# Performance work log

Measured on AMD Instinct MI355X. Metric: run time of the kernel, lower is better.

Reference implementation:

```python
import jax, jax.numpy as jnp
import numpy as np

EPS = 1e-6

def _mlp3(x, Wa, ba, Wb, bb, Wc, bc):
    h = jax.nn.relu(x @ Wa + ba)
    h = jax.nn.relu(h @ Wb + bb)
    return h @ Wc + bc

def setup_inputs() -> dict:
    key = jax.random.key(0)
    ks = jax.random.split(key, 16)
    B, D, C, N = 1024, 1024, 128, 100000
    s = 0.02  # weight scale
    return {
        "query": jax.random.normal(ks[0], (B, D), jnp.float32),
        "W1": jax.random.normal(ks[1], (D, D // 2), jnp.float32) * s,
        "b1": jnp.zeros((D // 2,), jnp.float32),
        "W2": jax.random.normal(ks[2], (D // 2, D // 4), jnp.float32) * s,
        "b2": jnp.zeros((D // 4,), jnp.float32),
        "W3": jax.random.normal(ks[3], (D // 4, C), jnp.float32) * s,
        "b3": jnp.zeros((C,), jnp.float32),
        "keys": jax.random.normal(ks[4], (N, C), jnp.float32),
        "values": jax.random.normal(ks[5], (N, C), jnp.float32),
        "D1w": jax.random.normal(ks[6], (C, D // 4), jnp.float32) * s,
        "D1b": jnp.zeros((D // 4,), jnp.float32),
        "D2w": jax.random.normal(ks[7], (D // 4, D // 2), jnp.float32) * s,
        "D2b": jnp.zeros((D // 2,), jnp.float32),
        "D3w": jax.random.normal(ks[8], (D // 2, D), jnp.float32) * s,
        "D3b": jnp.zeros((D,), jnp.float32),
        "k": 5,
    }

def reference(query, W1, b1, W2, b2, W3, b3, keys, values,
              D1w, D1b, D2w, D2b, D3w, D3b, k):
    # Compress query (FAISS path detaches, so stop_gradient is faithful)
    cq = _mlp3(query, W1, b1, W2, b2, W3, b3)          # [B, C]
    cq = jax.lax.stop_gradient(cq)
    keys_c = jax.lax.stop_gradient(keys)
    vals = jax.lax.stop_gradient(values)               # stored values were .detach()ed
    # Brute-force squared-L2 distances (IndexFlatL2 returns squared L2): [B, N]
    d2 = (jnp.sum(cq * cq, axis=1, keepdims=True)
          + jnp.sum(keys_c * keys_c, axis=1)[None, :]
          - 2.0 * cq @ keys_c.T)
    neg_d, idx = jax.lax.top_k(-d2, k)                 # k nearest, ascending distance
    dist = -neg_d                                      # [B, k]
    w = 1.0 / (dist + EPS)
    w = w / jnp.sum(w, axis=1, keepdims=True)          # [B, k]
    gathered = vals[idx]                               # [B, k, C]
    weighted = jnp.einsum('bk,bkc->bc', w, gathered)   # [B, C]
    retrieved = _mlp3(weighted, D1w, D1b, D2w, D2b, D3w, D3b)  # [B, D]
    confidence = 1.0 / (dist[:, 0] + EPS)              # [B]
    return retrieved, confidence
```

## Files before the change

### kernel.cpp

```cpp
#include <hip/hip_runtime.h>
#include <hip/hip_bf16.h>

#define NKEYS  100000
#define NCH    128
#define CHK    832
#define TPC    13
#define KPAD   (NCH * CHK)
#define NTILE  (KPAD / 64)
#define BQ     1024
#define EPS_F  1e-6f
#define NCAND  (NCH * 3)
#define BIGF   1e30f

typedef __attribute__((ext_vector_type(8))) short bf16x8;
typedef __attribute__((ext_vector_type(4))) float f32x4;

__device__ __forceinline__ void gl_lds16(const uint4* g, uint4* l) {
    __builtin_amdgcn_global_load_lds((const __attribute__((address_space(1))) void*)g,
                                     (__attribute__((address_space(3))) void*)l, 16, 0, 0);
}
__device__ __forceinline__ unsigned umn(unsigned a, unsigned b) { return a < b ? a : b; }
__device__ __forceinline__ unsigned umx(unsigned a, unsigned b) { return a > b ? a : b; }
__device__ __forceinline__ ushort bf16bits(float v) {
    __hip_bfloat16 h = __float2bfloat16(v);
    return *(ushort*)&h;
}

__device__ __forceinline__ void ins3u(unsigned (&m)[3], unsigned u) {
    unsigned v1 = umn(m[2], u);
    m[2] = umx(m[1], v1);
    unsigned v2 = umn(m[1], v1);
    m[1] = umx(m[0], v2);
    m[0] = umn(m[0], v2);
}

__device__ __forceinline__ void ins5(float (&d)[5], int (&ix)[5], float nd, int ni) {
    if (nd < d[4]) {
        d[4] = nd; ix[4] = ni;
#pragma unroll
        for (int p = 4; p > 0; --p) {
            if (d[p] < d[p - 1]) {
                float td = d[p]; d[p] = d[p - 1]; d[p - 1] = td;
                int   ti = ix[p]; ix[p] = ix[p - 1]; ix[p - 1] = ti;
            }
        }
    }
}

__global__ __launch_bounds__(256)
void cvt_keys(const float* __restrict__ keys, uint4* __restrict__ img,
              float* __restrict__ kk, float* __restrict__ khalf) {
    const int tid = threadIdx.x;
    const int r = tid >> 2, s = tid & 3;
    const int tile = blockIdx.x;
    const int n = tile * 64 + r;
    const int ct = r >> 4, l15 = r & 15;
    const bool live = (n < NKEYS);
    const float* kp = keys + (size_t)n * 128 + s * 32;
    float ss = 0.f;
    uint4 out[4];
#pragma unroll
    for (int q = 0; q < 4; ++q) {
        float4 a = make_float4(0.f, 0.f, 0.f, 0.f), b = a;
        if (live) { a = *(const float4*)(kp + q * 8); b = *(const float4*)(kp + q * 8 + 4); }
        ss += a.x * a.x + a.y * a.y + a.z * a.z + a.w * a.w
            + b.x * b.x + b.y * b.y + b.z * b.z + b.w * b.w;
        float v[8] = {a.x, a.y, a.z, a.w, b.x, b.y, b.z, b.w};
        ushort h[8];
#pragma unroll
        for (int j = 0; j < 8; ++j) h[j] = bf16bits(v[j]);
        out[q] = make_uint4((uint)h[0] | ((uint)h[1] << 16), (uint)h[2] | ((uint)h[3] << 16),
                            (uint)h[4] | ((uint)h[5] << 16), (uint)h[6] | ((uint)h[7] << 16));
    }
    ss += __shfl_xor(ss, 1, 64);
    ss += __shfl_xor(ss, 2, 64);
    if (s == 0) {
        kk[n]    = live ? ss : BIGF;
        khalf[n] = live ? -0.5f * ss : -BIGF;
    }
#pragma unroll
    for (int q = 0; q < 4; ++q)
        img[(size_t)tile * 1024 + ((ct * 4 + s) * 4 + q) * 16 + l15] = out[q];
}

__global__ __launch_bounds__(256)
void split_a(const float* __restrict__ A, ushort* __restrict__ Ax, int K) {
    const int row = blockIdx.x;
    for (int i = threadIdx.x * 4; i < K; i += 1024) {
        float4 v = *(const float4*)&A[(size_t)row * K + i];
        float x[4] = {v.x, v.y, v.z, v.w};
        ushort h[4], l[4];
#pragma unroll
        for (int j = 0; j < 4; ++j) {
            __hip_bfloat16 hb = __float2bfloat16(x[j]);
            h[j] = *(ushort*)&hb;
            l[j] = bf16bits(x[j] - __bfloat162float(hb));
        }
        ushort* o = Ax + (size_t)row * 3 * K;
        *(ushort4*)&o[i]         = make_ushort4(h[0], h[1], h[2], h[3]);
        *(ushort4*)&o[K + i]     = make_ushort4(l[0], l[1], l[2], l[3]);
        *(ushort4*)&o[2 * K + i] = make_ushort4(h[0], h[1], h[2], h[3]);
    }
}

__global__ __launch_bounds__(256)
void cvt_wT_split(const float* __restrict__ W, uint4* __restrict__ Wimg,
                  int Ksrc, int N) {
    const int ctile = blockIdx.x, p = blockIdx.y;
    const int npanT = gridDim.y;
    const int pk = Ksrc >> 6;
    const int part = p / pk, psrc = p - part * pk;
#pragma unroll
    for (int it = 0; it < 2; ++it) {
        int c = it * 256 + threadIdx.x;
        int l15 = c & 15, quad = (c >> 4) & 3, s = (c >> 6) & 1, ct = c >> 7;
        int n = ctile * 64 + ct * 16 + l15;
        int k = psrc * 64 + s * 32 + quad * 8;
        ushort h[8];
#pragma unroll
        for (int j = 0; j < 8; ++j) {
            float w = W[(size_t)(k + j) * N + n];
            __hip_bfloat16 hb = __float2bfloat16(w);
            if (part < 2) h[j] = *(ushort*)&hb;
            else h[j] = bf16bits(w - __bfloat162float(hb));
        }
        Wimg[((size_t)ctile * npanT + p) * 512 + c] =
            make_uint4((uint)h[0] | ((uint)h[1] << 16), (uint)h[2] | ((uint)h[3] << 16),
                       (uint)h[4] | ((uint)h[5] << 16), (uint)h[6] | ((uint)h[7] << 16));
    }
}

__global__ __launch_bounds__(256)
void bgemm_part(const ushort* __restrict__ Abf, const uint4* __restrict__ Wimg,
                float* __restrict__ P, int M, int N, int K, int ppz) {
    __shared__ uint4 pan[2][512];
    const int tid = threadIdx.x;
    const int wv = tid >> 6, ln = tid & 63;
    const int quad = ln >> 4, l15 = ln & 15;
    const int n0 = blockIdx.x * 64;
    const int m0 = blockIdx.y * 128 + wv * 32;
    const int ctile = blockIdx.x, npanT = K >> 6;
    const int p0 = blockIdx.z * ppz;
    f32x4 acc[2][4];
#pragma unroll
    for (int s = 0; s < 2; ++s)
#pragma unroll
        for (int c = 0; c < 4; ++c) acc[s][c] = (f32x4){0.f, 0.f, 0.f, 0.f};

#pragma unroll
    for (int it = 0; it < 2; ++it)
        gl_lds16(&Wimg[((size_t)ctile * npanT + p0) * 512 + it * 256 + wv * 64 + ln],
                 &pan[0][it * 256 + wv * 64]);
    __syncthreads();

    for (int pp = 0; pp < ppz; ++pp) {
        const int p = p0 + pp;
        const int b = pp & 1;
        if (pp + 1 < ppz) {
#pragma unroll
            for (int it = 0; it < 2; ++it)
                gl_lds16(&Wimg[((size_t)ctile * npanT + p + 1) * 512 + it * 256 + wv * 64 + ln],
                         &pan[b ^ 1][it * 256 + wv * 64]);
        }
        const ushort* arow = Abf + (size_t)(m0 + l15) * K + p * 64 + quad * 8;
        bf16x8 afA[2], afB[2];
#pragma unroll
        for (int s = 0; s < 2; ++s) {
            afA[s] = *(const bf16x8*)(arow + s * 32);
            afB[s] = *(const bf16x8*)(arow + (size_t)16 * K + s * 32);
        }
#pragma unroll
        for (int ct = 0; ct < 4; ++ct)
#pragma unroll
            for (int s = 0; s < 2; ++s) {
                bf16x8 bfr = *(const bf16x8*)&pan[b][((ct * 2 + s) * 4 + quad) * 16 + l15];
                acc[0][ct] = __builtin_amdgcn_mfma_f32_16x16x32_bf16(afA[s], bfr, acc[0][ct], 0, 0, 0);
                acc[1][ct] = __builtin_amdgcn_mfma_f32_16x16x32_bf16(afB[s], bfr, acc[1][ct], 0, 0, 0);
            }
        __syncthreads();
    }

    P += (size_t)blockIdx.z * M * N;
#pragma unroll
    for (int ct = 0; ct < 4; ++ct) {
        const int col = n0 + ct * 16 + l15;
#pragma unroll
        for (int set = 0; set < 2; ++set)
#pragma unroll
            for (int r = 0; r < 4; ++r)
                P[(size_t)(m0 + set * 16 + quad * 4 + r) * N + col] = acc[set][ct][r];
    }
}

template <int NP>
__global__ __launch_bounds__(256)
void sgemm_part(const float* __restrict__ A, const float* __restrict__ abias,
                const float* __restrict__ W, float* __restrict__ P,
                int M, int N, int K, int kslice, int MNpart) {
    __shared__ float As[16][68];
    __shared__ float Bs[16][64];
    const int tid = threadIdx.x;
    const int tx = tid & 15, ty = tid >> 4;
    const int m0 = blockIdx.y * 64, n0 = blockIdx.x * 64;
    const int kb = blockIdx.z * kslice, ke = kb + kslice;
    float acc[4][4] = {};
    for (int k0 = kb; k0 < ke; k0 += 16) {
        {
            int m = tid >> 2, k4 = (tid & 3) * 4;
            const float* ap = &A[(size_t)(m0 + m) * K + k0 + k4];
            float4 a = *(const float4*)ap;
            if (NP > 0) {
#pragma unroll
                for (int z = 1; z < NP; ++z) {
                    float4 v = *(const float4*)(ap + (size_t)z * MNpart);
                    a.x += v.x; a.y += v.y; a.z += v.z; a.w += v.w;
                }
                float4 b = *(const float4*)&abias[k0 + k4];
                a.x = fmaxf(a.x + b.x, 0.f); a.y = fmaxf(a.y + b.y, 0.f);
                a.z = fmaxf(a.z + b.z, 0.f); a.w = fmaxf(a.w + b.w, 0.f);
            }
            As[k4 + 0][m] = a.x; As[k4 + 1][m] = a.y;
            As[k4 + 2][m] = a.z; As[k4 + 3][m] = a.w;
        }
        {
            int k = tid >> 4, n4 = (tid & 15) * 4;
            *(float4*)&Bs[k][n4] = *(const float4*)&W[(size_t)(k0 + k) * N + n0 + n4];
        }
        __syncthreads();
#pragma unroll
        for (int kkk = 0; kkk < 16; ++kkk) {
            float4 a4 = *(const float4*)&As[kkk][ty * 4];
            float4 b4 = *(const float4*)&Bs[kkk][tx * 4];
            float av[4] = {a4.x, a4.y, a4.z, a4.w};
            float bv[4] = {b4.x, b4.y, b4.z, b4.w};
#pragma unroll
            for (int i = 0; i < 4; ++i)
#pragma unroll
                for (int j = 0; j < 4; ++j)
                    acc[i][j] = fmaf(av[i], bv[j], acc[i][j]);
        }
        __syncthreads();
    }
    P += (size_t)blockIdx.z * M * N;
#pragma unroll
    for (int i = 0; i < 4; ++i)
        *(float4*)&P[(size_t)(m0 + ty * 4 + i) * N + n0 + tx * 4] =
            make_float4(acc[i][0], acc[i][1], acc[i][2], acc[i][3]);
}

__global__ __launch_bounds__(128)
void final_row(const float* __restrict__ P, const float* __restrict__ bias,
               float* __restrict__ cq, ushort* __restrict__ qbf,
               float* __restrict__ qq) {
    __shared__ float red[2];
    const int row = blockIdx.x, c = threadIdx.x;
    float v = 0.f;
#pragma unroll
    for (int z = 0; z < 8; ++z) v += P[(size_t)z * (BQ * 128) + row * 128 + c];
    v += bias[c];
    cq[(size_t)row * 128 + c] = v;
    qbf[(size_t)row * 128 + c] = bf16bits(v);
    float s = v * v;
#pragma unroll
    for (int off = 32; off > 0; off >>= 1) s += __shfl_down(s, off, 64);
    if ((c & 63) == 0) red[c >> 6] = s;
    __syncthreads();
    if (c == 0) qq[row] = red[0] + red[1];
}

__device__ __forceinline__ void wT_panel(const float* __restrict__ W, uint4* __restrict__ Wimg,
                                         int K, int N, int ctile, int p) {
    const int npan = K >> 6;
#pragma unroll
    for (int it = 0; it < 2; ++it) {
        int c = it * 256 + threadIdx.x;
        int l15 = c & 15, quad = (c >> 4) & 3, s = (c >> 6) & 1, ct = c >> 7;
        int n = ctile * 64 + ct * 16 + l15;
        int k = p * 64 + s * 32 + quad * 8;
        ushort h[8];
#pragma unroll
        for (int j = 0; j < 8; ++j) h[j] = bf16bits(W[(size_t)(k + j) * N + n]);
        Wimg[((size_t)ctile * npan + p) * 512 + c] =
            make_uint4((uint)h[0] | ((uint)h[1] << 16), (uint)h[2] | ((uint)h[3] << 16),
                       (uint)h[4] | ((uint)h[5] << 16), (uint)h[6] | ((uint)h[7] << 16));
    }
}

__global__ __launch_bounds__(256)
void cvt_wT_all(const float* __restrict__ W1, const float* __restrict__ W2,
                const float* __restrict__ W3, uint4* __restrict__ I1,
                uint4* __restrict__ I2, uint4* __restrict__ I3) {
    int b = blockIdx.x;
    if (b < 8)       { wT_panel(W1, I1, 128, 256,  b >> 1, b & 1); }
    else if (b < 40) { b -= 8;  wT_panel(W2, I2, 256, 512,  b >> 2, b & 3); }
    else             { b -= 40; wT_panel(W3, I3, 512, 1024, b >> 3, b & 7); }
}

__global__ __launch_bounds__(512, 4)
void screen_topk(const ushort* __restrict__ qbf, const uint4* __restrict__ img,
                 const float* __restrict__ khalf, int* __restrict__ cand_i) {
    __shared__ uint4 buf[2][1024];
    __shared__ float kls[CHK];
    const int tid = threadIdx.x;
    const int wv = tid >> 6, ln = tid & 63;
    const int quad = ln >> 4, l15 = ln & 15;
    const int m0 = blockIdx.y * 256 + wv * 32;
    const int c0 = blockIdx.x * CHK;
    const int t0 = blockIdx.x * TPC;

    bf16x8 afA[4], afB[4];
    {
        const ushort* qa = qbf + (size_t)(m0 + l15) * 128 + quad * 8;
#pragma unroll
        for (int s = 0; s < 4; ++s) {
            afA[s] = *(const bf16x8*)(qa + 32 * s);
            afB[s] = *(const bf16x8*)(qa + 16 * 128 + 32 * s);
        }
    }
    for (int i = tid; i < CHK; i += 512) kls[i] = khalf[c0 + i];

    unsigned mA[4][3], mB[4][3];
#pragma unroll
    for (int r = 0; r < 4; ++r)
#pragma unroll
        for (int p = 0; p < 3; ++p) { mA[r][p] = 0xFFFFFFFFu; mB[r][p] = 0xFFFFFFFFu; }

#pragma unroll
    for (int it = 0; it < 2; ++it)
        gl_lds16(&img[(size_t)t0 * 1024 + it * 512 + wv * 64 + ln],
                 &buf[0][it * 512 + wv * 64]);
    __syncthreads();

    for (int t = 0; t < TPC; ++t) {
        const int b = t & 1;
        if (t + 1 < TPC) {
#pragma unroll
            for (int it = 0; it < 2; ++it)
                gl_lds16(&img[(size_t)(t0 + t + 1) * 1024 + it * 512 + wv * 64 + ln],
                         &buf[b ^ 1][it * 512 + wv * 64]);
        }
#pragma unroll
        for (int ct = 0; ct < 4; ++ct) {
            const int nl = t * 64 + ct * 16 + l15;
            const float kh = kls[nl];
            f32x4 a0 = {kh, kh, kh, kh}, a1 = {kh, kh, kh, kh};
#pragma unroll
            for (int s = 0; s < 4; ++s) {
                bf16x8 bfr = *(const bf16x8*)&buf[b][(ct * 4 + s) * 64 + ln];
                a0 = __builtin_amdgcn_mfma_f32_16x16x32_bf16(afA[s], bfr, a0, 0, 0, 0);
                a1 = __builtin_amdgcn_mfma_f32_16x16x32_bf16(afB[s], bfr, a1, 0, 0, 0);
            }
#pragma unroll
            for (int r = 0; r < 4; ++r) {
                ins3u(mA[r], (__float_as_uint(a0[r]) & 0xFFFFF800u) | (unsigned)nl);
                ins3u(mB[r], (__float_as_uint(a1[r]) & 0xFFFFF800u) | (unsigned)nl);
            }
        }
        __syncthreads();
    }

#pragma unroll
    for (int set = 0; set < 2; ++set) {
#pragma unroll
        for (int r = 0; r < 4; ++r) {
            unsigned m[3];
#pragma unroll
            for (int p = 0; p < 3; ++p) m[p] = set ? mB[r][p] : mA[r][p];
#pragma unroll
            for (int st = 1; st <= 8; st <<= 1) {
                unsigned o[3];
#pragma unroll
                for (int p = 0; p < 3; ++p) o[p] = (unsigned)__shfl_xor((int)m[p], st, 64);
#pragma unroll
                for (int p = 0; p < 3; ++p) ins3u(m, o[p]);
            }
            if (l15 == 0) {
                const int row = m0 + set * 16 + quad * 4 + r;
#pragma unroll
                for (int p = 0; p < 3; ++p)
                    cand_i[((size_t)row * NCH + blockIdx.x) * 3 + p] = c0 + (int)(m[p] & 0x7FFu);
            }
        }
    }
}

__global__ __launch_bounds__(512)
void rerank_gather(const int* __restrict__ cand_i, const float* __restrict__ cq,
                   const float* __restrict__ keysf, const float* __restrict__ qq,
                   const float* __restrict__ kk, const float* __restrict__ values,
                   ushort* __restrict__ wbf, float* __restrict__ conf_out) {
    __shared__ __align__(16) float qs[128];
    __shared__ float ed[NCAND];
    __shared__ int   ei[NCAND];
    __shared__ float w5[5];
    __shared__ int   s5[5];
    __shared__ float confs;
    const int row = blockIdx.x, tid = threadIdx.x;
    const int ln = tid & 63;
    const int qd = tid >> 4;
    const int l15 = tid & 15;
    if (tid < 128) qs[tid] = cq[(size_t)row * 128 + tid];
    for (int c = tid; c < NCAND; c += 512) ei[c] = cand_i[(size_t)row * NCAND + c];
    __syncthreads();
    const float4 qa = *(const float4*)&qs[l15 * 8];
    const float4 qb = *(const float4*)&qs[l15 * 8 + 4];
    const float qqr = qq[row];
#pragma unroll 3
    for (int it = 0; it < (NCAND + 31) / 32; ++it) {
        const int c = qd + it * 32;
        if (c < NCAND) {
            const int idx = ei[c];
            const int idc = idx < NKEYS ? idx : NKEYS - 1;
            const float* kp = &keysf[(size_t)idc * 128 + l15 * 8];
            const float4 ka = *(const float4*)kp;
            const float4 kb = *(const float4*)(kp + 4);
            float dot = qa.x * ka.x + qa.y * ka.y + qa.z * ka.z + qa.w * ka.w
                      + qb.x * kb.x + qb.y * kb.y + qb.z * kb.z + qb.w * kb.w;
            dot += __shfl_xor(dot, 1, 64);
            dot += __shfl_xor(dot, 2, 64);
            dot += __shfl_xor(dot, 4, 64);
            dot += __shfl_xor(dot, 8, 64);
            if (l15 == 0) ed[c] = qqr + kk[idx] - 2.0f * dot;
        }
    }
    __syncthreads();
    if (tid < 64) {
        float bd[5]; int bi[5];
#pragma unroll
        for (int p = 0; p < 5; ++p) { bd[p] = BIGF; bi[p] = 0; }
        for (int c = ln; c < NCAND; c += 64) ins5(bd, bi, ed[c], ei[c]);
#pragma unroll
        for (int m = 1; m <= 32; m <<= 1) {
            float od[5]; int oi[5];
#pragma unroll
            for (int p = 0; p < 5; ++p) {
                od[p] = __shfl_xor(bd[p], m, 64);
                oi[p] = __shfl_xor(bi[p], m, 64);
            }
#pragma unroll
            for (int p = 0; p < 5; ++p) ins5(bd, bi, od[p], oi[p]);
        }
        if (ln == 0) {
            float ww[5]; float s = 0.f;
#pragma unroll
            for (int p = 0; p < 5; ++p) { ww[p] = 1.0f / (bd[p] + EPS_F); s += ww[p]; }
#pragma unroll
            for (int p = 0; p < 5; ++p) { w5[p] = ww[p] / s; s5[p] = bi[p]; }
            confs = 1.0f / (bd[0] + EPS_F);
        }
    }
    __syncthreads();
    if (tid < 128) {
        float acc = 0.f;
#pragma unroll
        for (int p = 0; p < 5; ++p) acc += w5[p] * values[(size_t)s5[p] * 128 + tid];
        wbf[(size_t)row * 128 + tid] = bf16bits(acc);
    }
    if (tid == 0) conf_out[row] = confs;
}

template <int RELU, int OUTF32>
__global__ __launch_bounds__(256)
void bgemm_bias(const ushort* __restrict__ Abf, const uint4* __restrict__ Wimg,
                const float* __restrict__ bias, void* __restrict__ Cout,
                int M, int N, int K) {
    __shared__ uint4 pan[2][512];
    const int tid = threadIdx.x;
    const int wv = tid >> 6, ln = tid & 63;
    const int quad = ln >> 4, l15 = ln & 15;
    const int n0 = blockIdx.x * 64;
    const int m0 = blockIdx.y * 128 + wv * 32;
    const int ctile = blockIdx.x, npan = K >> 6;
    f32x4 acc[2][4];
#pragma unroll
    for (int s = 0; s < 2; ++s)
#pragma unroll
        for (int c = 0; c < 4; ++c) acc[s][c] = (f32x4){0.f, 0.f, 0.f, 0.f};

#pragma unroll
    for (int it = 0; it < 2; ++it)
        gl_lds16(&Wimg[(size_t)ctile * npan * 512 + it * 256 + wv * 64 + ln],
                 &pan[0][it * 256 + wv * 64]);
    __syncthreads();

    for (int p = 0; p < npan; ++p) {
        const int b = p & 1;
        if (p + 1 < npan) {
#pragma unroll
            for (int it = 0; it < 2; ++it)
                gl_lds16(&Wimg[((size_t)ctile * npan + p + 1) * 512 + it * 256 + wv * 64 + ln],
                         &pan[b ^ 1][it * 256 + wv * 64]);
        }
        const ushort* arow = Abf + (size_t)(m0 + l15) * K + p * 64 + quad * 8;
        bf16x8 afA[2], afB[2];
#pragma unroll
        for (int s = 0; s < 2; ++s) {
            afA[s] = *(const bf16x8*)(arow + s * 32);
            afB[s] = *(const bf16x8*)(arow + (size_t)16 * K + s * 32);
        }
#pragma unroll
        for (int ct = 0; ct < 4; ++ct)
#pragma unroll
            for (int s = 0; s < 2; ++s) {
                bf16x8 bfr = *(const bf16x8*)&pan[b][((ct * 2 + s) * 4 + quad) * 16 + l15];
                acc[0][ct] = __builtin_amdgcn_mfma_f32_16x16x32_bf16(afA[s], bfr, acc[0][ct], 0, 0, 0);
                acc[1][ct] = __builtin_amdgcn_mfma_f32_16x16x32_bf16(afB[s], bfr, acc[1][ct], 0, 0, 0);
            }
        __syncthreads();
    }

#pragma unroll
    for (int ct = 0; ct < 4; ++ct) {
        const int col = n0 + ct * 16 + l15;
        const float bv = bias[col];
#pragma unroll
        for (int set = 0; set < 2; ++set)
#pragma unroll
            for (int r = 0; r < 4; ++r) {
                float v = acc[set][ct][r] + bv;
                if (RELU) v = fmaxf(v, 0.f);
                const int row = m0 + set * 16 + quad * 4 + r;
                if (OUTF32) ((float*)Cout)[(size_t)row * N + col] = v;
                else        ((ushort*)Cout)[(size_t)row * N + col] = bf16bits(v);
            }
    }
}

extern "C" void kernel_launch(void* const* d_in, const int* in_sizes, int n_in,
                              void* d_out, int out_size, void* d_ws, size_t ws_size,
                              hipStream_t stream) {
    const float* query  = (const float*)d_in[0];
    const float* W1     = (const float*)d_in[1];
    const float* b1     = (const float*)d_in[2];
    const float* W2     = (const float*)d_in[3];
    const float* b2     = (const float*)d_in[4];
    const float* W3     = (const float*)d_in[5];
    const float* b3     = (const float*)d_in[6];
    const float* keys   = (const float*)d_in[7];
    const float* values = (const float*)d_in[8];
    const float* D1w    = (const float*)d_in[9];
    const float* D1b    = (const float*)d_in[10];
    const float* D2w    = (const float*)d_in[11];
    const float* D2b    = (const float*)d_in[12];
    const float* D3w    = (const float*)d_in[13];
    const float* D3b    = (const float*)d_in[14];
    float* out = (float*)d_out;

    float*  ws    = (float*)d_ws;
    float*  kk    = ws;
    float*  khalf = ws + 106496;
    float*  qq    = ws + 212992;
    float*  cq    = ws + 214016;
    ushort* qbf   = (ushort*)(ws + 345088);
    int*    cand  = (int*)(ws + 410624);
    float*  R     = ws + 803840;
    ushort* xbig  = (ushort*)R;
    uint4*  W1img = (uint4*)(R + 1572864);
    float*  partA = R + 2359296;
    float*  partB = R + 5505024;
    float*  partC = R + 7602176;
    uint4*  img   = (uint4*)R;
    ushort* wbf   = (ushort*)R;
    ushort* h3bf  = (ushort*)(R + 65536);
    ushort* h4bf  = (ushort*)(R + 196608);
    uint4*  Wimg1 = (uint4*)(R + 458752);
    uint4*  Wimg2 = (uint4*)(R + 475136);
    uint4*  Wimg3 = (uint4*)(R + 540672);
    float*  conf  = out + 1024 * 1024;

    split_a<<<1024, 256, 0, stream>>>(query, xbig, 1024);
    cvt_wT_split<<<dim3(8, 48), 256, 0, stream>>>(W1, W1img, 1024, 512);
    bgemm_part<<<dim3(8, 8, 6), 256, 0, stream>>>(xbig, W1img, partA, 1024, 512, 3072, 8);
    sgemm_part<6><<<dim3(4, 16, 8), 256, 0, stream>>>(partA, b1, W2, partB, 1024, 256, 512, 64, 1024 * 512);
    sgemm_part<8><<<dim3(2, 16, 8), 256, 0, stream>>>(partB, b2, W3, partC, 1024, 128, 256, 32, 1024 * 256);
    final_row<<<1024, 128, 0, stream>>>(partC, b3, cq, qbf, qq);
    cvt_keys<<<NTILE, 256, 0, stream>>>(keys, img, kk, khalf);
    screen_topk<<<dim3(NCH, BQ / 256), 512, 0, stream>>>(qbf, img, khalf, cand);
    rerank_gather<<<BQ, 512, 0, stream>>>(cand, cq, keys, qq, kk, values, wbf, conf);
    cvt_wT_all<<<168, 256, 0, stream>>>(D1w, D2w, D3w, Wimg1, Wimg2, Wimg3);
    bgemm_bias<1, 0><<<dim3(4, 8),  256, 0, stream>>>(wbf,  Wimg1, D1b, h3bf, 1024, 256,  128);
    bgemm_bias<1, 0><<<dim3(8, 8),  256, 0, stream>>>(h3bf, Wimg2, D2b, h4bf, 1024, 512,  256);
    bgemm_bias<0, 1><<<dim3(16, 8), 256, 0, stream>>>(h4bf, Wimg3, D3b, out,  1024, 1024, 512);

    (void)in_sizes; (void)n_in; (void)out_size; (void)ws_size;
}
```

Before: 284.1 us.

## Merge query/W1 prep kernels, retune chunking and split-K factors

Fuses the query split and W1 conversion kernels into a single prep launch to remove one launch. Changes key chunking from 128 chunks of 832 to 192 chunks of 576, giving the screen kernel more blocks and more candidates. Halves split-K depth for the second and third encoder GEMMs, with final_row now summing 4 partials instead of 8. The workspace offsets are moved to match the larger candidate buffer.

Result: slower. 295.1 us (+3.9%).

```diff
diff --git a/kernel.cpp b/kernel.cpp
--- a/kernel.cpp
+++ b/kernel.cpp
@@ -2,9 +2,9 @@
 #include <hip/hip_bf16.h>
 
 #define NKEYS  100000
-#define NCH    128
-#define CHK    832
-#define TPC    13
+#define NCH    192
+#define CHK    576
+#define TPC    9
 #define KPAD   (NCH * CHK)
 #define NTILE  (KPAD / 64)
 #define BQ     1024
@@ -84,10 +84,13 @@
 }
 
 __global__ __launch_bounds__(256)
-void split_a(const float* __restrict__ A, ushort* __restrict__ Ax, int K) {
-    const int row = blockIdx.x;
-    for (int i = threadIdx.x * 4; i < K; i += 1024) {
-        float4 v = *(const float4*)&A[(size_t)row * K + i];
+void prep(const float* __restrict__ A, ushort* __restrict__ Ax,
+          const float* __restrict__ W, uint4* __restrict__ Wimg) {
+    const int b = blockIdx.x;
+    if (b < 1024) {
+        const int row = b;
+        const int i = threadIdx.x * 4;
+        float4 v = *(const float4*)&A[(size_t)row * 1024 + i];
         float x[4] = {v.x, v.y, v.z, v.w};
         ushort h[4], l[4];
 #pragma unroll
@@ -96,37 +99,32 @@
             h[j] = *(ushort*)&hb;
             l[j] = bf16bits(x[j] - __bfloat162float(hb));
         }
-        ushort* o = Ax + (size_t)row * 3 * K;
-        *(ushort4*)&o[i]         = make_ushort4(h[0], h[1], h[2], h[3]);
-        *(ushort4*)&o[K + i]     = make_ushort4(l[0], l[1], l[2], l[3]);
-        *(ushort4*)&o[2 * K + i] = make_ushort4(h[0], h[1], h[2], h[3]);
-    }
-}
-
-__global__ __launch_bounds__(256)
-void cvt_wT_split(const float* __restrict__ W, uint4* __restrict__ Wimg,
-                  int Ksrc, int N) {
-    const int ctile = blockIdx.x, p = blockIdx.y;
-    const int npanT = gridDim.y;
-    const int pk = Ksrc >> 6;
-    const int part = p / pk, psrc = p - part * pk;
-#pragma unroll
-    for (int it = 0; it < 2; ++it) {
-        int c = it * 256 + threadIdx.x;
-        int l15 = c & 15, quad = (c >> 4) & 3, s = (c >> 6) & 1, ct = c >> 7;
-        int n = ctile * 64 + ct * 16 + l15;
-        int k = psrc * 64 + s * 32 + quad * 8;
-        ushort h[8];
-#pragma unroll
-        for (int j = 0; j < 8; ++j) {
-            float w = W[(size_t)(k + j) * N + n];
-            __hip_bfloat16 hb = __float2bfloat16(w);
-            if (part < 2) h[j] = *(ushort*)&hb;
-            else h[j] = bf16bits(w - __bfloat162float(hb));
-        }
-        Wimg[((size_t)ctile * npanT + p) * 512 + c] =
-            make_uint4((uint)h[0] | ((uint)h[1] << 16), (uint)h[2] | ((uint)h[3] << 16),
-                       (uint)h[4] | ((uint)h[5] << 16), (uint)h[6] | ((uint)h[7] << 16));
+        ushort* o = Ax + (size_t)row * 3072;
+        *(ushort4*)&o[i]        = make_ushort4(h[0], h[1], h[2], h[3]);
+        *(ushort4*)&o[1024 + i] = make_ushort4(l[0], l[1], l[2], l[3]);
+        *(ushort4*)&o[2048 + i] = make_ushort4(h[0], h[1], h[2], h[3]);
+    } else {
+        const int idx = b - 1024;
+        const int ctile = idx / 48, p = idx % 48;
+        const int part = p >> 4, psrc = p & 15;
+#pragma unroll
+        for (int it = 0; it < 2; ++it) {
+            int c = it * 256 + threadIdx.x;
+            int l15 = c & 15, quad = (c >> 4) & 3, s = (c >> 6) & 1, ct = c >> 7;
+            int n = ctile * 64 + ct * 16 + l15;
+            int k = psrc * 64 + s * 32 + quad * 8;
+            ushort h[8];
+#pragma unroll
+            for (int j = 0; j < 8; ++j) {
+                float w = W[(size_t)(k + j) * 512 + n];
+                __hip_bfloat16 hb = __float2bfloat16(w);
+                if (part < 2) h[j] = *(ushort*)&hb;
+                else h[j] = bf16bits(w - __bfloat162float(hb));
+            }
+            Wimg[((size_t)ctile * 48 + p) * 512 + c] =
+                make_uint4((uint)h[0] | ((uint)h[1] << 16), (uint)h[2] | ((uint)h[3] << 16),
+                           (uint)h[4] | ((uint)h[5] << 16), (uint)h[6] | ((uint)h[7] << 16));
+        }
     }
 }
 
@@ -256,7 +254,7 @@
     const int row = blockIdx.x, c = threadIdx.x;
     float v = 0.f;
 #pragma unroll
-    for (int z = 0; z < 8; ++z) v += P[(size_t)z * (BQ * 128) + row * 128 + c];
+    for (int z = 0; z < 4; ++z) v += P[(size_t)z * (BQ * 128) + row * 128 + c];
     v += bias[c];
     cq[(size_t)row * 128 + c] = v;
     qbf[(size_t)row * 128 + c] = bf16bits(v);
@@ -548,17 +546,17 @@
 
     float*  ws    = (float*)d_ws;
     float*  kk    = ws;
-    float*  khalf = ws + 106496;
-    float*  qq    = ws + 212992;
-    float*  cq    = ws + 214016;
-    ushort* qbf   = (ushort*)(ws + 345088);
-    int*    cand  = (int*)(ws + 410624);
-    float*  R     = ws + 803840;
+    float*  khalf = ws + 110592;
+    float*  qq    = ws + 221184;
+    float*  cq    = ws + 222208;
+    ushort* qbf   = (ushort*)(ws + 353280);
+    int*    cand  = (int*)(ws + 418816);
+    float*  R     = ws + 1008640;
     ushort* xbig  = (ushort*)R;
     uint4*  W1img = (uint4*)(R + 1572864);
     float*  partA = R + 2359296;
     float*  partB = R + 5505024;
-    float*  partC = R + 7602176;
+    float*  partC = R + 6553600;
     uint4*  img   = (uint4*)R;
     ushort* wbf   = (ushort*)R;
     ushort* h3bf  = (ushort*)(R + 65536);
@@ -568,11 +566,10 @@
     uint4*  Wimg3 = (uint4*)(R + 540672);
     float*  conf  = out + 1024 * 1024;
 
-    split_a<<<1024, 256, 0, stream>>>(query, xbig, 1024);
-    cvt_wT_split<<<dim3(8, 48), 256, 0, stream>>>(W1, W1img, 1024, 512);
+    prep<<<1408, 256, 0, stream>>>(query, xbig, W1, W1img);
     bgemm_part<<<dim3(8, 8, 6), 256, 0, stream>>>(xbig, W1img, partA, 1024, 512, 3072, 8);
-    sgemm_part<6><<<dim3(4, 16, 8), 256, 0, stream>>>(partA, b1, W2, partB, 1024, 256, 512, 64, 1024 * 512);
-    sgemm_part<8><<<dim3(2, 16, 8), 256, 0, stream>>>(partB, b2, W3, partC, 1024, 128, 256, 32, 1024 * 256);
+    sgemm_part<6><<<dim3(4, 16, 4), 256, 0, stream>>>(partA, b1, W2, partB, 1024, 256, 512, 128, 1024 * 512);
+    sgemm_part<4><<<dim3(2, 16, 4), 256, 0, stream>>>(partB, b2, W3, partC, 1024, 128, 256, 64, 1024 * 256);
     final_row<<<1024, 128, 0, stream>>>(partC, b3, cq, qbf, qq);
     cvt_keys<<<NTILE, 256, 0, stream>>>(keys, img, kk, khalf);
     screen_topk<<<dim3(NCH, BQ / 256), 512, 0, stream>>>(qbf, img, khalf, cand);
```
